# Optimization experiments

Measured on AMD Instinct MI355X. Metric: run time of the kernel, lower is better.

Reference implementation:

```python
import jax, jax.numpy as jnp
import numpy as np

WS = 8        # window_size
SHIFT = 4     # shift_size
NH = 6        # num_heads
EPS = 1e-5


def _rel_pos_index(ws):
    coords = np.stack(np.meshgrid(np.arange(ws), np.arange(ws), indexing='ij'))  # [2,ws,ws]
    cf = coords.reshape(2, -1)                      # [2, ws*ws]
    rel = cf[:, :, None] - cf[:, None, :]           # [2, N, N]
    rel = rel.transpose(1, 2, 0)                    # [N, N, 2]
    rel[:, :, 0] += ws - 1
    rel[:, :, 1] += ws - 1
    rel[:, :, 0] *= 2 * ws - 1
    return rel.sum(-1)                              # [N, N] int


def _attn_mask(H, W, ws, shift):
    img = np.zeros((H, W), dtype=np.float32)
    slices = (slice(0, -ws), slice(-ws, -shift), slice(-shift, None))
    cnt = 0
    for hs in slices:
        for wsl in slices:
            img[hs, wsl] = cnt
            cnt += 1
    mw = img.reshape(H // ws, ws, W // ws, ws).transpose(0, 2, 1, 3).reshape(-1, ws * ws)
    diff = mw[:, None, :] - mw[:, :, None]          # [nW, N, N]
    return np.where(diff != 0, -100.0, 0.0).astype(np.float32)


def _layernorm(x, g, b):
    mu = x.mean(-1, keepdims=True)
    var = ((x - mu) ** 2).mean(-1, keepdims=True)
    return (x - mu) * jax.lax.rsqrt(var + EPS) * g + b


def setup_inputs() -> dict:
    key = jax.random.key(0)
    ks = jax.random.split(key, 8)
    C, HID = 192, 768
    return {
        'x': jax.random.normal(ks[0], (8, 128, 128, C), jnp.float32),
        'g1': jnp.ones((C,), jnp.float32),
        'b1': jnp.zeros((C,), jnp.float32),
        'qkv_w': jax.random.normal(ks[1], (3 * C, C), jnp.float32) * 0.02,
        'qkv_b': jnp.zeros((3 * C,), jnp.float32),
        'rpb_table': jax.random.normal(ks[2], ((2 * WS - 1) ** 2, NH), jnp.float32) * 0.02,
        'proj_w': jax.random.normal(ks[3], (C, C), jnp.float32) * 0.02,
        'proj_b': jnp.zeros((C,), jnp.float32),
        'g2': jnp.ones((C,), jnp.float32),
        'b2': jnp.zeros((C,), jnp.float32),
        'fc1_w': jax.random.normal(ks[4], (HID, C), jnp.float32) * 0.02,
        'fc1_b': jnp.zeros((HID,), jnp.float32),
        'fc2_w': jax.random.normal(ks[5], (C, HID), jnp.float32) * 0.02,
        'fc2_b': jnp.zeros((C,), jnp.float32),
    }


def reference(x, g1, b1, qkv_w, qkv_b, rpb_table, proj_w, proj_b, g2, b2,
              fc1_w, fc1_b, fc2_w, fc2_b):
    B, H, W, C = x.shape
    N = WS * WS
    hd = C // NH
    scale = hd ** -0.5

    rpi = jnp.asarray(_rel_pos_index(WS))                 # [N,N] static
    mask = jnp.asarray(_attn_mask(H, W, WS, SHIFT))       # [nW,N,N] static
    nW = mask.shape[0]

    shortcut = x.reshape(B, H * W, C)
    xn = _layernorm(shortcut, g1, b1).reshape(B, H, W, C)

    # cyclic shift
    xs = jnp.roll(xn, shift=(-SHIFT, -SHIFT), axis=(1, 2))

    # window partition -> [B*nW, N, C]
    win = xs.reshape(B, H // WS, WS, W // WS, WS, C).transpose(0, 1, 3, 2, 4, 5)
    win = win.reshape(-1, N, C)
    B_ = win.shape[0]

    # qkv
    qkv = jnp.einsum('bnc,oc->bno', win, qkv_w) + qkv_b   # [B_,N,3C]
    qkv = qkv.reshape(B_, N, 3, NH, hd).transpose(2, 0, 3, 1, 4)  # [3,B_,NH,N,hd]
    q, k, v = qkv[0] * scale, qkv[1], qkv[2]

    attn = jnp.einsum('bhnd,bhmd->bhnm', q, k)            # [B_,NH,N,N]
    bias = rpb_table[rpi.reshape(-1)].reshape(N, N, NH).transpose(2, 0, 1)
    attn = attn + bias[None]
    attn = attn.reshape(B, nW, NH, N, N) + mask[None, :, None]
    attn = jax.nn.softmax(attn.reshape(B_, NH, N, N), axis=-1)

    out = jnp.einsum('bhnm,bhmd->bhnd', attn, v)          # [B_,NH,N,hd]
    out = out.transpose(0, 2, 1, 3).reshape(B_, N, C)
    out = jnp.einsum('bnc,oc->bno', out, proj_w) + proj_b

    # window reverse -> [B,H,W,C]
    out = out.reshape(B, H // WS, W // WS, WS, WS, C).transpose(0, 1, 3, 2, 4, 5)
    out = out.reshape(B, H, W, C)
    out = jnp.roll(out, shift=(SHIFT, SHIFT), axis=(1, 2)).reshape(B, H * W, C)

    x1 = shortcut + out
    h = _layernorm(x1, g2, b2)
    h = jnp.einsum('bnc,hc->bnh', h, fc1_w) + fc1_b
    h = jax.nn.gelu(h, approximate=False)
    h = jnp.einsum('bnh,ch->bnc', h, fc2_w) + fc2_b
    x2 = x1 + h
    return x2.reshape(B, H, W, C)
```

## Files before the change

kernel.cpp:

```cpp
#include <hip/hip_runtime.h>
#include <hip/hip_bf16.h>

typedef __attribute__((ext_vector_type(8))) short s16x8;
typedef __attribute__((ext_vector_type(4))) float f32x4;

#define TOK 131072

__device__ __forceinline__ unsigned short f2bf(float f){
    __hip_bfloat16 h = __float2bfloat16(f);
    return *reinterpret_cast<unsigned short*>(&h);
}

__device__ __forceinline__ int flab(int g){ return (g < 120) ? 0 : ((g < 124) ? 1 : 2); }

__device__ __forceinline__ void async16(const void* g, void* l){
    __builtin_amdgcn_global_load_lds(
        (const __attribute__((address_space(1))) unsigned int*)g,
        (__attribute__((address_space(3))) unsigned int*)l, 16, 0, 0);
}

__global__ __launch_bounds__(256) void wconv_all(
    const float* __restrict__ w0, const float* __restrict__ w1,
    const float* __restrict__ w2, const float* __restrict__ w3,
    unsigned short* __restrict__ o0, unsigned short* __restrict__ o1,
    unsigned short* __restrict__ o2, unsigned short* __restrict__ o3)
{
    int i = blockIdx.x*256 + threadIdx.x;
    if (i < 110592) o0[i] = f2bf(w0[i]);
    if (i < 36864)  o1[i] = f2bf(w1[i]);
    if (i < 147456) o2[i] = f2bf(w2[i]);
    if (i < 147456) o3[i] = f2bf(w3[i]);
}

__global__ __launch_bounds__(256) void ln1_win_kernel(
    const float* __restrict__ x, const float* __restrict__ g,
    const float* __restrict__ b, unsigned short* __restrict__ win)
{
    int wid  = blockIdx.x*4 + (threadIdx.x >> 6);
    int lane = threadIdx.x & 63;
    int b_ = wid >> 6, n = wid & 63;
    int bb = b_ >> 8, wi = b_ & 255;
    int wh = wi >> 4, ww = wi & 15;
    int r = n >> 3, c = n & 7;
    int h = (wh*8 + r + 4) & 127;
    int w = (ww*8 + c + 4) & 127;
    const float* px = x + (((size_t)bb*128 + h)*128 + w)*192;
    float v0 = px[lane], v1 = px[lane+64], v2 = px[lane+128];
    float s = v0 + v1 + v2;
    #pragma unroll
    for (int o = 1; o < 64; o <<= 1) s += __shfl_xor(s, o);
    float mu = s * (1.0f/192.0f);
    float d0 = v0-mu, d1 = v1-mu, d2 = v2-mu;
    float qv = d0*d0 + d1*d1 + d2*d2;
    #pragma unroll
    for (int o = 1; o < 64; o <<= 1) qv += __shfl_xor(qv, o);
    float rstd = rsqrtf(qv * (1.0f/192.0f) + 1e-5f);
    unsigned short* pw = win + (size_t)wid*192;
    pw[lane]     = f2bf(d0*rstd*g[lane]     + b[lane]);
    pw[lane+64]  = f2bf(d1*rstd*g[lane+64]  + b[lane+64]);
    pw[lane+128] = f2bf(d2*rstd*g[lane+128] + b[lane+128]);
}

__global__ __launch_bounds__(256) void ln2_kernel(
    const float* __restrict__ x1, const float* __restrict__ g,
    const float* __restrict__ b, unsigned short* __restrict__ out)
{
    int t = blockIdx.x*4 + (threadIdx.x >> 6);
    int lane = threadIdx.x & 63;
    const float* px = x1 + (size_t)t*192;
    float v0 = px[lane], v1 = px[lane+64], v2 = px[lane+128];
    float s = v0 + v1 + v2;
    #pragma unroll
    for (int o = 1; o < 64; o <<= 1) s += __shfl_xor(s, o);
    float mu = s * (1.0f/192.0f);
    float d0 = v0-mu, d1 = v1-mu, d2 = v2-mu;
    float qv = d0*d0 + d1*d1 + d2*d2;
    #pragma unroll
    for (int o = 1; o < 64; o <<= 1) qv += __shfl_xor(qv, o);
    float rstd = rsqrtf(qv * (1.0f/192.0f) + 1e-5f);
    unsigned short* pw = out + (size_t)t*192;
    pw[lane]     = f2bf(d0*rstd*g[lane]     + b[lane]);
    pw[lane+64]  = f2bf(d1*rstd*g[lane+64]  + b[lane+64]);
    pw[lane+128] = f2bf(d2*rstd*g[lane+128] + b[lane+128]);
}

__device__ __forceinline__ void mm256x64(
    const unsigned short* __restrict__ A, const unsigned short* __restrict__ W,
    int K, int m0, int o0, unsigned short* As, unsigned short* Bs,
    f32x4 (&acc)[4][4])
{
    const int tid = threadIdx.x, wv = tid >> 6, lane = tid & 63;
    const int lrow = lane & 15, quad = lane >> 4;
    const int lr8 = lane >> 3, lb = lane & 7;
    const int sb = ((lb ^ lr8) << 3);
    #pragma unroll
    for (int i = 0; i < 4; ++i)
        #pragma unroll
        for (int j = 0; j < 4; ++j) acc[i][j] = (f32x4){0.f,0.f,0.f,0.f};

    const unsigned short* Abase = A + (size_t)(m0 + wv*8 + lr8)*K + sb;
    const unsigned short* Wbase = W + (size_t)(o0 + wv*8 + lr8)*K + sb;

    for (int k0 = 0; k0 < K; k0 += 64) {
        #pragma unroll
        for (int it = 0; it < 8; ++it)
            async16(Abase + (size_t)(it*32)*K + k0, As + (it*4 + wv)*512);
        #pragma unroll
        for (int it = 0; it < 2; ++it)
            async16(Wbase + (size_t)(it*32)*K + k0, Bs + (it*4 + wv)*512);
        __syncthreads();
        #pragma unroll
        for (int kc = 0; kc < 2; ++kc) {
            const int blk = quad + 4*kc;
            s16x8 af[4], bf[4];
            #pragma unroll
            for (int i = 0; i < 4; ++i) {
                int row = wv*64 + i*16 + lrow;
                af[i] = *(const s16x8*)(As + row*64 + ((blk ^ (row & 7)) << 3));
            }
            #pragma unroll
            for (int j = 0; j < 4; ++j) {
                int row = j*16 + lrow;
                bf[j] = *(const s16x8*)(Bs + row*64 + ((blk ^ (row & 7)) << 3));
            }
            #pragma unroll
            for (int i = 0; i < 4; ++i)
                #pragma unroll
                for (int j = 0; j < 4; ++j)
                    acc[i][j] = __builtin_amdgcn_mfma_f32_16x16x32_bf16(af[i], bf[j], acc[i][j], 0, 0, 0);
        }
        __syncthreads();
    }
}

__global__ __launch_bounds__(256) void gemm_qkv_kernel(
    const unsigned short* __restrict__ A, const unsigned short* __restrict__ Wm,
    const float* __restrict__ bias, unsigned short* __restrict__ qo,
    unsigned short* __restrict__ ko, unsigned short* __restrict__ vo)
{
    __shared__ __attribute__((aligned(16))) char smem[40960];
    unsigned short* As = (unsigned short*)smem;
    unsigned short* Bs = (unsigned short*)(smem + 32768);
    const int m0 = blockIdx.y*256, o0 = blockIdx.x*64;
    f32x4 acc[4][4];
    mm256x64(A, Wm, 192, m0, o0, As, Bs, acc);
    const int tid = threadIdx.x, wv = tid >> 6, lane = tid & 63;
    const int lrow = lane & 15, quad = lane >> 4;
    const int part = o0 / 192;
    float bv[4];
    #pragma unroll
    for (int j = 0; j < 4; ++j) bv[j] = bias[o0 + j*16 + lrow];

    if (part < 2) {
        unsigned short* dst = (part == 0) ? qo : ko;
        const float scale = (part == 0) ? 0.17677669529663687f : 1.0f;
        unsigned short* T = (unsigned short*)smem;
        #pragma unroll
        for (int i = 0; i < 4; ++i)
            #pragma unroll
            for (int j = 0; j < 4; ++j)
                #pragma unroll
                for (int rg = 0; rg < 4; ++rg) {
                    int ml = wv*64 + i*16 + quad*4 + rg;
                    T[ml*72 + j*16 + lrow] = f2bf((acc[i][j][rg] + bv[j]) * scale);
                }
        __syncthreads();
        for (int c = tid; c < 2048; c += 256) {
            int row = c >> 3, blk = c & 7;
            int m = m0 + row, b_ = m >> 6, n = m & 63;
            int o_in = o0 + blk*8 - part*192;
            int head = o_in >> 5, d = o_in & 31;
            *(int4*)(dst + ((size_t)(b_*6 + head)*64 + n)*32 + d) =
                *(const int4*)(T + row*72 + blk*8);
        }
    } else {
        unsigned short* T = (unsigned short*)smem;
        #pragma unroll
        for (int i = 0; i < 4; ++i)
            #pragma unroll
            for (int j = 0; j < 4; ++j)
                #pragma unroll
                for (int rg = 0; rg < 4; ++rg) {
                    int ml = wv*64 + i*16 + quad*4 + rg;
                    T[(j*16 + lrow)*264 + ml] = f2bf(acc[i][j][rg] + bv[j]);
                }
        __syncthreads();
        for (int c = tid; c < 2048; c += 256) {
            int col = c >> 5, mb = c & 31;
            int b_ = (m0 >> 6) + (mb >> 3), n = (mb & 7) * 8;
            int o_in = o0 + col - 384;
            int head = o_in >> 5, d = o_in & 31;
            *(int4*)(vo + ((size_t)(b_*6 + head)*32 + d)*64 + n) =
                *(const int4*)(T + col*264 + mb*8);
        }
    }
}

__global__ __launch_bounds__(384) void attn_kernel(
    const unsigned short* __restrict__ q, const unsigned short* __restrict__ k,
    const unsigned short* __restrict__ vT, const float* __restrict__ rpb,
    unsigned short* __restrict__ ao)
{
    __shared__ float rpb_s[1350];
    __shared__ __attribute__((aligned(16))) unsigned short p_lds[6*4608];
    const int b_ = blockIdx.x;
    const int h = threadIdx.x >> 6;
    const int lane = threadIdx.x & 63, lrow = lane & 15, quad = lane >> 4;
    for (int i = threadIdx.x; i < 1350; i += 384) rpb_s[i] = rpb[i];
    __syncthreads();

    const size_t hb = ((size_t)b_*6 + h)*2048;
    const unsigned short* qb = q  + hb;
    const unsigned short* kb = k  + hb;
    const unsigned short* vb = vT + hb;

    s16x8 qf[4], kf[4];
    #pragma unroll
    for (int i = 0; i < 4; ++i) qf[i] = *(const s16x8*)(qb + (i*16+lrow)*32 + quad*8);
    #pragma unroll
    for (int j = 0; j < 4; ++j) kf[j] = *(const s16x8*)(kb + (j*16+lrow)*32 + quad*8);

    const f32x4 zz = {0.f,0.f,0.f,0.f};
    f32x4 s[4][4];
    #pragma unroll
    for (int i = 0; i < 4; ++i)
        #pragma unroll
        for (int j = 0; j < 4; ++j)
            s[i][j] = __builtin_amdgcn_mfma_f32_16x16x32_bf16(qf[i], kf[j], zz, 0, 0, 0);

    const int wi = b_ & 255, wh = wi >> 4, ww = wi & 15;
    int labm[4];
    #pragma unroll
    for (int j = 0; j < 4; ++j) {
        int m = j*16 + lrow;
        labm[j] = flab(wh*8 + (m >> 3))*3 + flab(ww*8 + (m & 7));
    }
    unsigned short* pl = p_lds + h*4608;
    #pragma unroll
    for (int i = 0; i < 4; ++i) {
        #pragma unroll
        for (int rg = 0; rg < 4; ++rg) {
            int n = i*16 + quad*4 + rg;
            int rn = n >> 3, cn = n & 7;
            int labn = flab(wh*8 + rn)*3 + flab(ww*8 + cn);
            float vals[4];
            float vmax = -1e30f;
            #pragma unroll
            for (int j = 0; j < 4; ++j) {
                int m = j*16 + lrow;
                int idx = ((rn - (m >> 3) + 7)*15 + (cn - (m & 7) + 7))*6 + h;
                float val = s[i][j][rg] + rpb_s[idx];
                if (labn != labm[j]) val -= 100.f;
                vals[j] = val;
                vmax = fmaxf(vmax, val);
            }
            #pragma unroll
            for (int o = 1; o < 16; o <<= 1) vmax = fmaxf(vmax, __shfl_xor(vmax, o));
            float sum = 0.f;
            #pragma unroll
            for (int j = 0; j < 4; ++j) { vals[j] = __expf(vals[j] - vmax); sum += vals[j]; }
            #pragma unroll
            for (int o = 1; o < 16; o <<= 1) sum += __shfl_xor(sum, o);
            float inv = 1.f / sum;
            #pragma unroll
            for (int j = 0; j < 4; ++j) pl[n*72 + j*16 + lrow] = f2bf(vals[j]*inv);
        }
    }
    __syncthreads();

    f32x4 oacc[4][2];
    #pragma unroll
    for (int i = 0; i < 4; ++i) { oacc[i][0] = zz; oacc[i][1] = zz; }
    #pragma unroll
    for (int kc = 0; kc < 2; ++kc) {
        s16x8 vf[2];
        #pragma unroll
        for (int jd = 0; jd < 2; ++jd)
            vf[jd] = *(const s16x8*)(vb + (jd*16+lrow)*64 + kc*32 + quad*8);
        #pragma unroll
        for (int i = 0; i < 4; ++i) {
            s16x8 pf = *(const s16x8*)(pl + (i*16+lrow)*72 + kc*32 + quad*8);
            #pragma unroll
            for (int jd = 0; jd < 2; ++jd)
                oacc[i][jd] = __builtin_amdgcn_mfma_f32_16x16x32_bf16(pf, vf[jd], oacc[i][jd], 0, 0, 0);
        }
    }
    unsigned short* ob = ao + (size_t)b_*12288 + h*32;
    #pragma unroll
    for (int i = 0; i < 4; ++i)
        #pragma unroll
        for (int jd = 0; jd < 2; ++jd)
            #pragma unroll
            for (int rg = 0; rg < 4; ++rg) {
                int n = i*16 + quad*4 + rg;
                ob[(size_t)n*192 + jd*16 + lrow] = f2bf(oacc[i][jd][rg]);
            }
}

__global__ __launch_bounds__(256) void gemm_proj_kernel(
    const unsigned short* __restrict__ A, const unsigned short* __restrict__ Wm,
    const float* __restrict__ bias, const float* __restrict__ x, float* __restrict__ x1)
{
    __shared__ __attribute__((aligned(16))) char smem[40960];
    unsigned short* As = (unsigned short*)smem;
    unsigned short* Bs = (unsigned short*)(smem + 32768);
    const int m0 = blockIdx.y*256, o0 = blockIdx.x*64;
    f32x4 acc[4][4];
    mm256x64(A, Wm, 192, m0, o0, As, Bs, acc);
    const int tid = threadIdx.x, wv = tid >> 6, lane = tid & 63;
    const int lrow = lane & 15, quad = lane >> 4;
    float bv[4];
    #pragma unroll
    for (int j = 0; j < 4; ++j) bv[j] = bias[o0 + j*16 + lrow];
    float* T = (float*)smem;
    #pragma unroll
    for (int pass = 0; pass < 2; ++pass) {
        __syncthreads();
        if ((wv >> 1) == pass) {
            int wl = wv & 1;
            #pragma unroll
            for (int i = 0; i < 4; ++i)
                #pragma unroll
                for (int j = 0; j < 4; ++j)
                    #pragma unroll
                    for (int rg = 0; rg < 4; ++rg)
                        T[(wl*64 + i*16 + quad*4 + rg)*68 + j*16 + lrow] = acc[i][j][rg] + bv[j];
        }
        __syncthreads();
        for (int c = tid; c < 2048; c += 256) {
            int row = c >> 4, blk = c & 15;
            int m = m0 + pass*128 + row;
            int b_ = m >> 6, n = m & 63;
            int bb = b_ >> 8, wi = b_ & 255, wh = wi >> 4, ww = wi & 15;
            int r = n >> 3, cc = n & 7;
            int hh = (wh*8 + r + 4) & 127;
            int wwp = (ww*8 + cc + 4) & 127;
            size_t addr = (((size_t)bb*128 + hh)*128 + wwp)*192 + o0 + blk*4;
            float4 v = *(const float4*)(T + row*68 + blk*4);
            float4 rx = *(const float4*)(x + addr);
            v.x += rx.x; v.y += rx.y; v.z += rx.z; v.w += rx.w;
            *(float4*)(x1 + addr) = v;
        }
    }
}

__global__ __launch_bounds__(256) void gemm_fc1_kernel(
    const unsigned short* __restrict__ A, const unsigned short* __restrict__ Wm,
    const float* __restrict__ bias, unsigned short* __restrict__ h1)
{
    __shared__ __attribute__((aligned(16))) char smem[40960];
    unsigned short* As = (unsigned short*)smem;
    unsigned short* Bs = (unsigned short*)(smem + 32768);
    const int m0 = blockIdx.y*256, o0 = blockIdx.x*64;
    f32x4 acc[4][4];
    mm256x64(A, Wm, 192, m0, o0, As, Bs, acc);
    const int tid = threadIdx.x, wv = tid >> 6, lane = tid & 63;
    const int lrow = lane & 15, quad = lane >> 4;
    float bv[4];
    #pragma unroll
    for (int j = 0; j < 4; ++j) bv[j] = bias[o0 + j*16 + lrow];
    unsigned short* T = (unsigned short*)smem;
    #pragma unroll
    for (int i = 0; i < 4; ++i)
        #pragma unroll
        for (int j = 0; j < 4; ++j)
            #pragma unroll
            for (int rg = 0; rg < 4; ++rg) {
                int ml = wv*64 + i*16 + quad*4 + rg;
                float v = acc[i][j][rg] + bv[j];
                v = 0.5f * v * (1.0f + erff(v * 0.7071067811865475f));
                T[ml*72 + j*16 + lrow] = f2bf(v);
            }
    __syncthreads();
    for (int c = tid; c < 2048; c += 256) {
        int row = c >> 3, blk = c & 7;
        *(int4*)(h1 + (size_t)(m0 + row)*768 + o0 + blk*8) =
            *(const int4*)(T + row*72 + blk*8);
    }
}

__global__ __launch_bounds__(256) void gemm_fc2_kernel(
    const unsigned short* __restrict__ A, const unsigned short* __restrict__ Wm,
    const float* __restrict__ bias, const float* __restrict__ x1, float* __restrict__ out)
{
    __shared__ __attribute__((aligned(16))) char smem[40960];
    unsigned short* As = (unsigned short*)smem;
    unsigned short* Bs = (unsigned short*)(smem + 32768);
    const int m0 = blockIdx.y*256, o0 = blockIdx.x*64;
    f32x4 acc[4][4];
    mm256x64(A, Wm, 768, m0, o0, As, Bs, acc);
    const int tid = threadIdx.x, wv = tid >> 6, lane = tid & 63;
    const int lrow = lane & 15, quad = lane >> 4;
    float bv[4];
    #pragma unroll
    for (int j = 0; j < 4; ++j) bv[j] = bias[o0 + j*16 + lrow];
    float* T = (float*)smem;
    #pragma unroll
    for (int pass = 0; pass < 2; ++pass) {
        __syncthreads();
        if ((wv >> 1) == pass) {
            int wl = wv & 1;
            #pragma unroll
            for (int i = 0; i < 4; ++i)
                #pragma unroll
                for (int j = 0; j < 4; ++j)
                    #pragma unroll
                    for (int rg = 0; rg < 4; ++rg)
                        T[(wl*64 + i*16 + quad*4 + rg)*68 + j*16 + lrow] = acc[i][j][rg] + bv[j];
        }
        __syncthreads();
        for (int c = tid; c < 2048; c += 256) {
            int row = c >> 4, blk = c & 15;
            size_t addr = (size_t)(m0 + pass*128 + row)*192 + o0 + blk*4;
            float4 v = *(const float4*)(T + row*68 + blk*4);
            float4 rx = *(const float4*)(x1 + addr);
            v.x += rx.x; v.y += rx.y; v.z += rx.z; v.w += rx.w;
            *(float4*)(out + addr) = v;
        }
    }
}

extern "C" void kernel_launch(void* const* d_in, const int* in_sizes, int n_in,
                              void* d_out, int out_size, void* d_ws, size_t ws_size,
                              hipStream_t stream)
{
    const float* x      = (const float*)d_in[0];
    const float* g1     = (const float*)d_in[1];
    const float* b1     = (const float*)d_in[2];
    const float* qkv_w  = (const float*)d_in[3];
    const float* qkv_b  = (const float*)d_in[4];
    const float* rpb    = (const float*)d_in[5];
    const float* proj_w = (const float*)d_in[6];
    const float* proj_b = (const float*)d_in[7];
    const float* g2     = (const float*)d_in[8];
    const float* b2     = (const float*)d_in[9];
    const float* fc1_w  = (const float*)d_in[10];
    const float* fc1_b  = (const float*)d_in[11];
    const float* fc2_w  = (const float*)d_in[12];
    const float* fc2_b  = (const float*)d_in[13];
    float* out = (float*)d_out;
    char* ws = (char*)d_ws;

    if (ws_size < 353206272ULL) return;

    unsigned short* win  = (unsigned short*)(ws + 0);
    unsigned short* qbuf = (unsigned short*)(ws + 50331648);
    unsigned short* kbuf = (unsigned short*)(ws + 100663296);
    unsigned short* vbuf = (unsigned short*)(ws + 150994944);
    unsigned short* attn = (unsigned short*)(ws + 201326592);
    float*          x1   = (float*)        (ws + 251658240);
    unsigned short* wq   = (unsigned short*)(ws + 352321536);
    unsigned short* wp   = (unsigned short*)(ws + 352321536 + 221184);
    unsigned short* w1   = (unsigned short*)(ws + 352321536 + 221184 + 73728);
    unsigned short* w2   = (unsigned short*)(ws + 352321536 + 221184 + 73728 + 294912);
    unsigned short* h1   = (unsigned short*)(ws + 0);
    unsigned short* xln2 = attn;

    wconv_all<<<576, 256, 0, stream>>>(qkv_w, proj_w, fc1_w, fc2_w, wq, wp, w1, w2);
    ln1_win_kernel<<<TOK/4, 256, 0, stream>>>(x, g1, b1, win);
    gemm_qkv_kernel<<<dim3(9, 512), 256, 0, stream>>>(win, wq, qkv_b, qbuf, kbuf, vbuf);
    attn_kernel<<<2048, 384, 0, stream>>>(qbuf, kbuf, vbuf, rpb, attn);
    gemm_proj_kernel<<<dim3(3, 512), 256, 0, stream>>>(attn, wp, proj_b, x, x1);
    ln2_kernel<<<TOK/4, 256, 0, stream>>>(x1, g2, b2, xln2);
    gemm_fc1_kernel<<<dim3(12, 512), 256, 0, stream>>>(xln2, w1, fc1_b, h1);
    gemm_fc2_kernel<<<dim3(3, 512), 256, 0, stream>>>(h1, w2, fc2_b, x1, out);
}
```

Measured before the change: 673.5 us.

## Fuse LayerNorm1 into QKV GEMM and LayerNorm2 into projection GEMM

LN1 plus the window gather now run inside a per-window QKV kernel that keeps the normalized tile in LDS, so the separate `win` buffer round trip goes away. The projection kernel now covers all 192 output columns per window, which lets it add the residual, compute LN2 in registers and write both x1 and xln2. This removes the standalone ln2 pass. The FC1 and FC2 GEMMs switch to 128-row tiles for more blocks. The trade-offs are plain int4 global loads instead of async LDS loads in the fused kernels and more register pressure (acc[12] plus the LN vectors).

New measurement: 591.3 us. -12.2%, faster.

```diff
diff --git a/kernel.cpp b/kernel.cpp
--- a/kernel.cpp
+++ b/kernel.cpp
@@ -3,8 +3,6 @@
 
 typedef __attribute__((ext_vector_type(8))) short s16x8;
 typedef __attribute__((ext_vector_type(4))) float f32x4;
-
-#define TOK 131072
 
 __device__ __forceinline__ unsigned short f2bf(float f){
     __hip_bfloat16 h = __float2bfloat16(f);
@@ -32,166 +30,115 @@
     if (i < 147456) o3[i] = f2bf(w3[i]);
 }
 
-__global__ __launch_bounds__(256) void ln1_win_kernel(
-    const float* __restrict__ x, const float* __restrict__ g,
-    const float* __restrict__ b, unsigned short* __restrict__ win)
-{
-    int wid  = blockIdx.x*4 + (threadIdx.x >> 6);
-    int lane = threadIdx.x & 63;
-    int b_ = wid >> 6, n = wid & 63;
-    int bb = b_ >> 8, wi = b_ & 255;
-    int wh = wi >> 4, ww = wi & 15;
-    int r = n >> 3, c = n & 7;
-    int h = (wh*8 + r + 4) & 127;
-    int w = (ww*8 + c + 4) & 127;
-    const float* px = x + (((size_t)bb*128 + h)*128 + w)*192;
-    float v0 = px[lane], v1 = px[lane+64], v2 = px[lane+128];
-    float s = v0 + v1 + v2;
-    #pragma unroll
-    for (int o = 1; o < 64; o <<= 1) s += __shfl_xor(s, o);
-    float mu = s * (1.0f/192.0f);
-    float d0 = v0-mu, d1 = v1-mu, d2 = v2-mu;
-    float qv = d0*d0 + d1*d1 + d2*d2;
-    #pragma unroll
-    for (int o = 1; o < 64; o <<= 1) qv += __shfl_xor(qv, o);
-    float rstd = rsqrtf(qv * (1.0f/192.0f) + 1e-5f);
-    unsigned short* pw = win + (size_t)wid*192;
-    pw[lane]     = f2bf(d0*rstd*g[lane]     + b[lane]);
-    pw[lane+64]  = f2bf(d1*rstd*g[lane+64]  + b[lane+64]);
-    pw[lane+128] = f2bf(d2*rstd*g[lane+128] + b[lane+128]);
-}
-
-__global__ __launch_bounds__(256) void ln2_kernel(
-    const float* __restrict__ x1, const float* __restrict__ g,
-    const float* __restrict__ b, unsigned short* __restrict__ out)
-{
-    int t = blockIdx.x*4 + (threadIdx.x >> 6);
-    int lane = threadIdx.x & 63;
-    const float* px = x1 + (size_t)t*192;
-    float v0 = px[lane], v1 = px[lane+64], v2 = px[lane+128];
-    float s = v0 + v1 + v2;
-    #pragma unroll
-    for (int o = 1; o < 64; o <<= 1) s += __shfl_xor(s, o);
-    float mu = s * (1.0f/192.0f);
-    float d0 = v0-mu, d1 = v1-mu, d2 = v2-mu;
-    float qv = d0*d0 + d1*d1 + d2*d2;
-    #pragma unroll
-    for (int o = 1; o < 64; o <<= 1) qv += __shfl_xor(qv, o);
-    float rstd = rsqrtf(qv * (1.0f/192.0f) + 1e-5f);
-    unsigned short* pw = out + (size_t)t*192;
-    pw[lane]     = f2bf(d0*rstd*g[lane]     + b[lane]);
-    pw[lane+64]  = f2bf(d1*rstd*g[lane+64]  + b[lane+64]);
-    pw[lane+128] = f2bf(d2*rstd*g[lane+128] + b[lane+128]);
-}
-
-__device__ __forceinline__ void mm256x64(
-    const unsigned short* __restrict__ A, const unsigned short* __restrict__ W,
-    int K, int m0, int o0, unsigned short* As, unsigned short* Bs,
-    f32x4 (&acc)[4][4])
-{
-    const int tid = threadIdx.x, wv = tid >> 6, lane = tid & 63;
-    const int lrow = lane & 15, quad = lane >> 4;
-    const int lr8 = lane >> 3, lb = lane & 7;
-    const int sb = ((lb ^ lr8) << 3);
-    #pragma unroll
-    for (int i = 0; i < 4; ++i)
-        #pragma unroll
-        for (int j = 0; j < 4; ++j) acc[i][j] = (f32x4){0.f,0.f,0.f,0.f};
-
-    const unsigned short* Abase = A + (size_t)(m0 + wv*8 + lr8)*K + sb;
-    const unsigned short* Wbase = W + (size_t)(o0 + wv*8 + lr8)*K + sb;
-
-    for (int k0 = 0; k0 < K; k0 += 64) {
-        #pragma unroll
-        for (int it = 0; it < 8; ++it)
-            async16(Abase + (size_t)(it*32)*K + k0, As + (it*4 + wv)*512);
-        #pragma unroll
-        for (int it = 0; it < 2; ++it)
-            async16(Wbase + (size_t)(it*32)*K + k0, Bs + (it*4 + wv)*512);
-        __syncthreads();
-        #pragma unroll
-        for (int kc = 0; kc < 2; ++kc) {
-            const int blk = quad + 4*kc;
-            s16x8 af[4], bf[4];
-            #pragma unroll
-            for (int i = 0; i < 4; ++i) {
-                int row = wv*64 + i*16 + lrow;
-                af[i] = *(const s16x8*)(As + row*64 + ((blk ^ (row & 7)) << 3));
-            }
-            #pragma unroll
-            for (int j = 0; j < 4; ++j) {
-                int row = j*16 + lrow;
-                bf[j] = *(const s16x8*)(Bs + row*64 + ((blk ^ (row & 7)) << 3));
-            }
-            #pragma unroll
-            for (int i = 0; i < 4; ++i)
+__global__ __launch_bounds__(256) void lnqkv_kernel(
+    const float* __restrict__ x, const float* __restrict__ g1, const float* __restrict__ b1,
+    const unsigned short* __restrict__ wq, const float* __restrict__ qkvb,
+    unsigned short* __restrict__ qo, unsigned short* __restrict__ ko,
+    unsigned short* __restrict__ vo)
+{
+    __shared__ __attribute__((aligned(16))) unsigned short win[64*200];
+    __shared__ __attribute__((aligned(16))) unsigned short Bs[64*200];
+    const int b_ = blockIdx.x;
+    const int bb = b_>>8, wi = b_&255, wh = wi>>4, ww = wi&15;
+    const int tid = threadIdx.x;
+    const int wv = tid>>6, lane = tid&63, lrow = lane&15, quad = lane>>4;
+
+    {
+        const int n = tid>>2, q4 = tid&3;
+        const int r = n>>3, c = n&7;
+        const int hh = (wh*8 + r + 4)&127, wp = (ww*8 + c + 4)&127;
+        const float* px = x + (((size_t)bb*128+hh)*128+wp)*192 + q4*48;
+        float v[48];
+        #pragma unroll
+        for (int m=0;m<12;++m) *(float4*)(v+m*4) = *(const float4*)(px+m*4);
+        float s = 0.f;
+        #pragma unroll
+        for (int k=0;k<48;++k) s += v[k];
+        s += __shfl_xor(s,1); s += __shfl_xor(s,2);
+        float mu = s*(1.0f/192.0f);
+        float qv = 0.f;
+        #pragma unroll
+        for (int k=0;k<48;++k){ float d=v[k]-mu; qv += d*d; }
+        qv += __shfl_xor(qv,1); qv += __shfl_xor(qv,2);
+        float rstd = rsqrtf(qv*(1.0f/192.0f) + 1e-5f);
+        const float* pg = g1 + q4*48;
+        const float* pb = b1 + q4*48;
+        unsigned short* pw = win + n*200 + q4*48;
+        #pragma unroll
+        for (int k=0;k<48;++k) pw[k] = f2bf((v[k]-mu)*rstd*pg[k] + pb[k]);
+    }
+    __syncthreads();
+
+    s16x8 af[6];
+    #pragma unroll
+    for (int kc=0;kc<6;++kc)
+        af[kc] = *(const s16x8*)(win + (wv*16+lrow)*200 + kc*32 + quad*8);
+
+    for (int ot=0; ot<9; ++ot) {
+        const int o0 = ot*64;
+        __syncthreads();
+        #pragma unroll
+        for (int t=0;t<6;++t) {
+            int cid = tid + t*256;
+            *(int4*)(Bs + (cid/24)*200 + (cid%24)*8) =
+                *(const int4*)(wq + (size_t)o0*192 + cid*8);
+        }
+        __syncthreads();
+        f32x4 acc[4];
+        #pragma unroll
+        for (int j=0;j<4;++j) acc[j] = (f32x4){0.f,0.f,0.f,0.f};
+        #pragma unroll
+        for (int kc=0;kc<6;++kc)
+            #pragma unroll
+            for (int j=0;j<4;++j) {
+                s16x8 bf = *(const s16x8*)(Bs + (j*16+lrow)*200 + kc*32 + quad*8);
+                acc[j] = __builtin_amdgcn_mfma_f32_16x16x32_bf16(af[kc], bf, acc[j], 0, 0, 0);
+            }
+        __syncthreads();
+        unsigned short* T = Bs;
+        const int part = ot/3;
+        float bv[4];
+        #pragma unroll
+        for (int j=0;j<4;++j) bv[j] = qkvb[o0 + j*16 + lrow];
+
+        if (part < 2) {
+            const float scale = (part==0) ? 0.17677669529663687f : 1.0f;
+            #pragma unroll
+            for (int j=0;j<4;++j)
                 #pragma unroll
-                for (int j = 0; j < 4; ++j)
-                    acc[i][j] = __builtin_amdgcn_mfma_f32_16x16x32_bf16(af[i], bf[j], acc[i][j], 0, 0, 0);
-        }
-        __syncthreads();
-    }
-}
-
-__global__ __launch_bounds__(256) void gemm_qkv_kernel(
-    const unsigned short* __restrict__ A, const unsigned short* __restrict__ Wm,
-    const float* __restrict__ bias, unsigned short* __restrict__ qo,
-    unsigned short* __restrict__ ko, unsigned short* __restrict__ vo)
-{
-    __shared__ __attribute__((aligned(16))) char smem[40960];
-    unsigned short* As = (unsigned short*)smem;
-    unsigned short* Bs = (unsigned short*)(smem + 32768);
-    const int m0 = blockIdx.y*256, o0 = blockIdx.x*64;
-    f32x4 acc[4][4];
-    mm256x64(A, Wm, 192, m0, o0, As, Bs, acc);
-    const int tid = threadIdx.x, wv = tid >> 6, lane = tid & 63;
-    const int lrow = lane & 15, quad = lane >> 4;
-    const int part = o0 / 192;
-    float bv[4];
-    #pragma unroll
-    for (int j = 0; j < 4; ++j) bv[j] = bias[o0 + j*16 + lrow];
-
-    if (part < 2) {
-        unsigned short* dst = (part == 0) ? qo : ko;
-        const float scale = (part == 0) ? 0.17677669529663687f : 1.0f;
-        unsigned short* T = (unsigned short*)smem;
-        #pragma unroll
-        for (int i = 0; i < 4; ++i)
-            #pragma unroll
-            for (int j = 0; j < 4; ++j)
+                for (int rg=0;rg<4;++rg) {
+                    int n2 = wv*16 + quad*4 + rg;
+                    T[n2*72 + j*16 + lrow] = f2bf((acc[j][rg]+bv[j])*scale);
+                }
+            __syncthreads();
+            unsigned short* dst = (part==0) ? qo : ko;
+            #pragma unroll
+            for (int t=0;t<2;++t) {
+                int c = tid + t*256;
+                int n2 = c>>3, blk = c&7;
+                int o_in = o0 + blk*8 - part*192;
+                int head = o_in>>5, d = o_in&31;
+                *(int4*)(dst + (((size_t)b_*6+head)*64 + n2)*32 + d) =
+                    *(const int4*)(T + n2*72 + blk*8);
+            }
+        } else {
+            #pragma unroll
+            for (int j=0;j<4;++j)
                 #pragma unroll
-                for (int rg = 0; rg < 4; ++rg) {
-                    int ml = wv*64 + i*16 + quad*4 + rg;
-                    T[ml*72 + j*16 + lrow] = f2bf((acc[i][j][rg] + bv[j]) * scale);
+                for (int rg=0;rg<4;++rg) {
+                    int n2 = wv*16 + quad*4 + rg;
+                    T[(j*16+lrow)*72 + n2] = f2bf(acc[j][rg]+bv[j]);
                 }
-        __syncthreads();
-        for (int c = tid; c < 2048; c += 256) {
-            int row = c >> 3, blk = c & 7;
-            int m = m0 + row, b_ = m >> 6, n = m & 63;
-            int o_in = o0 + blk*8 - part*192;
-            int head = o_in >> 5, d = o_in & 31;
-            *(int4*)(dst + ((size_t)(b_*6 + head)*64 + n)*32 + d) =
-                *(const int4*)(T + row*72 + blk*8);
-        }
-    } else {
-        unsigned short* T = (unsigned short*)smem;
-        #pragma unroll
-        for (int i = 0; i < 4; ++i)
-            #pragma unroll
-            for (int j = 0; j < 4; ++j)
-                #pragma unroll
-                for (int rg = 0; rg < 4; ++rg) {
-                    int ml = wv*64 + i*16 + quad*4 + rg;
-                    T[(j*16 + lrow)*264 + ml] = f2bf(acc[i][j][rg] + bv[j]);
-                }
-        __syncthreads();
-        for (int c = tid; c < 2048; c += 256) {
-            int col = c >> 5, mb = c & 31;
-            int b_ = (m0 >> 6) + (mb >> 3), n = (mb & 7) * 8;
-            int o_in = o0 + col - 384;
-            int head = o_in >> 5, d = o_in & 31;
-            *(int4*)(vo + ((size_t)(b_*6 + head)*32 + d)*64 + n) =
-                *(const int4*)(T + col*264 + mb*8);
+            __syncthreads();
+            #pragma unroll
+            for (int t=0;t<2;++t) {
+                int c = tid + t*256;
+                int ol = c>>3, nb = (c&7)*8;
+                int o_in = o0 + ol - 384;
+                int head = o_in>>5, d = o_in&31;
+                *(int4*)(vo + (((size_t)b_*6+head)*32 + d)*64 + nb) =
+                    *(const int4*)(T + ol*72 + nb);
+            }
         }
     }
 }
@@ -297,50 +244,146 @@
             }
 }
 
-__global__ __launch_bounds__(256) void gemm_proj_kernel(
-    const unsigned short* __restrict__ A, const unsigned short* __restrict__ Wm,
-    const float* __restrict__ bias, const float* __restrict__ x, float* __restrict__ x1)
-{
-    __shared__ __attribute__((aligned(16))) char smem[40960];
+__global__ __launch_bounds__(256) void projln_kernel(
+    const unsigned short* __restrict__ A, const unsigned short* __restrict__ W,
+    const float* __restrict__ pbias, const float* __restrict__ x,
+    const float* __restrict__ g2, const float* __restrict__ b2,
+    float* __restrict__ x1, unsigned short* __restrict__ xln2)
+{
+    __shared__ __attribute__((aligned(16))) char smem[36864];
     unsigned short* As = (unsigned short*)smem;
-    unsigned short* Bs = (unsigned short*)(smem + 32768);
-    const int m0 = blockIdx.y*256, o0 = blockIdx.x*64;
-    f32x4 acc[4][4];
-    mm256x64(A, Wm, 192, m0, o0, As, Bs, acc);
-    const int tid = threadIdx.x, wv = tid >> 6, lane = tid & 63;
-    const int lrow = lane & 15, quad = lane >> 4;
-    float bv[4];
-    #pragma unroll
-    for (int j = 0; j < 4; ++j) bv[j] = bias[o0 + j*16 + lrow];
-    float* T = (float*)smem;
-    #pragma unroll
-    for (int pass = 0; pass < 2; ++pass) {
-        __syncthreads();
-        if ((wv >> 1) == pass) {
-            int wl = wv & 1;
-            #pragma unroll
-            for (int i = 0; i < 4; ++i)
+    unsigned short* Bs = (unsigned short*)(smem + 9216);
+    const int b_ = blockIdx.x;
+    const int tid = threadIdx.x, wv = tid>>6, lane = tid&63;
+    const int lrow = lane&15, quad = lane>>4;
+    const size_t m0 = (size_t)b_*64;
+
+    f32x4 acc[12];
+    #pragma unroll
+    for (int j=0;j<12;++j) acc[j] = (f32x4){0.f,0.f,0.f,0.f};
+
+    for (int k0=0;k0<192;k0+=64) {
+        __syncthreads();
+        #pragma unroll
+        for (int t=0;t<2;++t) {
+            int cid = tid + t*256;
+            *(int4*)(As + (cid>>3)*72 + (cid&7)*8) =
+                *(const int4*)(A + (m0 + (cid>>3))*192 + k0 + (cid&7)*8);
+        }
+        #pragma unroll
+        for (int t=0;t<6;++t) {
+            int cid = tid + t*256;
+            *(int4*)(Bs + (cid>>3)*72 + (cid&7)*8) =
+                *(const int4*)(W + (size_t)(cid>>3)*192 + k0 + (cid&7)*8);
+        }
+        __syncthreads();
+        #pragma unroll
+        for (int kc=0;kc<2;++kc) {
+            s16x8 af = *(const s16x8*)(As + (wv*16+lrow)*72 + kc*32 + quad*8);
+            #pragma unroll
+            for (int j=0;j<12;++j) {
+                s16x8 bf = *(const s16x8*)(Bs + (j*16+lrow)*72 + kc*32 + quad*8);
+                acc[j] = __builtin_amdgcn_mfma_f32_16x16x32_bf16(af, bf, acc[j], 0, 0, 0);
+            }
+        }
+    }
+    __syncthreads();
+
+    const int bb = b_>>8, wi = b_&255, wh = wi>>4, ww = wi&15;
+    float bv[12], gv[12], b2v[12];
+    #pragma unroll
+    for (int j=0;j<12;++j) {
+        bv[j]  = pbias[j*16+lrow];
+        gv[j]  = g2[j*16+lrow];
+        b2v[j] = b2[j*16+lrow];
+    }
+    unsigned short* T = (unsigned short*)smem;
+    #pragma unroll
+    for (int rg=0;rg<4;++rg) {
+        int n2 = wv*16 + quad*4 + rg;
+        int r = n2>>3, c = n2&7;
+        int hh = (wh*8+r+4)&127, wp = (ww*8+c+4)&127;
+        size_t tok = ((size_t)bb*128+hh)*128 + wp;
+        float xv[12];
+        float s = 0.f;
+        #pragma unroll
+        for (int j=0;j<12;++j) {
+            float t = acc[j][rg] + bv[j] + x[tok*192 + j*16 + lrow];
+            xv[j] = t; s += t;
+        }
+        #pragma unroll
+        for (int o=1;o<16;o<<=1) s += __shfl_xor(s, o);
+        float mu = s*(1.0f/192.0f);
+        float qv = 0.f;
+        #pragma unroll
+        for (int j=0;j<12;++j){ float d = xv[j]-mu; qv += d*d; }
+        #pragma unroll
+        for (int o=1;o<16;o<<=1) qv += __shfl_xor(qv, o);
+        float rstd = rsqrtf(qv*(1.0f/192.0f) + 1e-5f);
+        #pragma unroll
+        for (int j=0;j<12;++j) {
+            x1[tok*192 + j*16 + lrow] = xv[j];
+            T[n2*200 + j*16 + lrow] = f2bf((xv[j]-mu)*rstd*gv[j] + b2v[j]);
+        }
+    }
+    __syncthreads();
+    #pragma unroll
+    for (int t=0;t<6;++t) {
+        int cid = tid + t*256;
+        int n2 = cid/24, blk = cid%24;
+        int r = n2>>3, c = n2&7;
+        int hh = (wh*8+r+4)&127, wp = (ww*8+c+4)&127;
+        size_t tok = ((size_t)bb*128+hh)*128 + wp;
+        *(int4*)(xln2 + tok*192 + blk*8) = *(const int4*)(T + n2*200 + blk*8);
+    }
+}
+
+__device__ __forceinline__ void mm128x64(
+    const unsigned short* __restrict__ A, const unsigned short* __restrict__ W,
+    int K, size_t m0, int o0, unsigned short* As, unsigned short* Bs,
+    f32x4 (&acc)[2][4])
+{
+    const int tid = threadIdx.x, wv = tid>>6, lane = tid&63;
+    const int lrow = lane&15, quad = lane>>4;
+    const int lr8 = lane>>3, lb = lane&7;
+    const int sb = ((lb ^ lr8) << 3);
+    #pragma unroll
+    for (int i=0;i<2;++i)
+        #pragma unroll
+        for (int j=0;j<4;++j) acc[i][j] = (f32x4){0.f,0.f,0.f,0.f};
+
+    const unsigned short* Abase = A + (m0 + wv*8 + lr8)*K + sb;
+    const unsigned short* Wbase = W + (size_t)(o0 + wv*8 + lr8)*K + sb;
+
+    for (int k0=0;k0<K;k0+=64) {
+        #pragma unroll
+        for (int it=0;it<4;++it)
+            async16(Abase + (size_t)(it*32)*K + k0, As + (it*4+wv)*512);
+        #pragma unroll
+        for (int it=0;it<2;++it)
+            async16(Wbase + (size_t)(it*32)*K + k0, Bs + (it*4+wv)*512);
+        __syncthreads();
+        #pragma unroll
+        for (int kc=0;kc<2;++kc) {
+            const int blk = quad + 4*kc;
+            s16x8 af[2], bf[4];
+            #pragma unroll
+            for (int i=0;i<2;++i) {
+                int row = wv*32 + i*16 + lrow;
+                af[i] = *(const s16x8*)(As + row*64 + ((blk ^ (row&7)) << 3));
+            }
+            #pragma unroll
+            for (int j=0;j<4;++j) {
+                int row = j*16 + lrow;
+                bf[j] = *(const s16x8*)(Bs + row*64 + ((blk ^ (row&7)) << 3));
+            }
+            #pragma unroll
+            for (int i=0;i<2;++i)
                 #pragma unroll
-                for (int j = 0; j < 4; ++j)
-                    #pragma unroll
-                    for (int rg = 0; rg < 4; ++rg)
-                        T[(wl*64 + i*16 + quad*4 + rg)*68 + j*16 + lrow] = acc[i][j][rg] + bv[j];
-        }
-        __syncthreads();
-        for (int c = tid; c < 2048; c += 256) {
-            int row = c >> 4, blk = c & 15;
-            int m = m0 + pass*128 + row;
-            int b_ = m >> 6, n = m & 63;
-            int bb = b_ >> 8, wi = b_ & 255, wh = wi >> 4, ww = wi & 15;
-            int r = n >> 3, cc = n & 7;
-            int hh = (wh*8 + r + 4) & 127;
-            int wwp = (ww*8 + cc + 4) & 127;
-            size_t addr = (((size_t)bb*128 + hh)*128 + wwp)*192 + o0 + blk*4;
-            float4 v = *(const float4*)(T + row*68 + blk*4);
-            float4 rx = *(const float4*)(x + addr);
-            v.x += rx.x; v.y += rx.y; v.z += rx.z; v.w += rx.w;
-            *(float4*)(x1 + addr) = v;
-        }
+                for (int j=0;j<4;++j)
+                    acc[i][j] = __builtin_amdgcn_mfma_f32_16x16x32_bf16(af[i], bf[j], acc[i][j], 0, 0, 0);
+        }
+        __syncthreads();
     }
 }
 
@@ -348,34 +391,36 @@
     const unsigned short* __restrict__ A, const unsigned short* __restrict__ Wm,
     const float* __restrict__ bias, unsigned short* __restrict__ h1)
 {
-    __shared__ __attribute__((aligned(16))) char smem[40960];
+    __shared__ __attribute__((aligned(16))) char smem[24576];
     unsigned short* As = (unsigned short*)smem;
-    unsigned short* Bs = (unsigned short*)(smem + 32768);
-    const int m0 = blockIdx.y*256, o0 = blockIdx.x*64;
-    f32x4 acc[4][4];
-    mm256x64(A, Wm, 192, m0, o0, As, Bs, acc);
-    const int tid = threadIdx.x, wv = tid >> 6, lane = tid & 63;
-    const int lrow = lane & 15, quad = lane >> 4;
+    unsigned short* Bs = (unsigned short*)(smem + 16384);
+    const size_t m0 = (size_t)blockIdx.y*128;
+    const int o0 = blockIdx.x*64;
+    f32x4 acc[2][4];
+    mm128x64(A, Wm, 192, m0, o0, As, Bs, acc);
+    const int tid = threadIdx.x, wv = tid>>6, lane = tid&63;
+    const int lrow = lane&15, quad = lane>>4;
     float bv[4];
     #pragma unroll
-    for (int j = 0; j < 4; ++j) bv[j] = bias[o0 + j*16 + lrow];
+    for (int j=0;j<4;++j) bv[j] = bias[o0 + j*16 + lrow];
     unsigned short* T = (unsigned short*)smem;
     #pragma unroll
-    for (int i = 0; i < 4; ++i)
-        #pragma unroll
-        for (int j = 0; j < 4; ++j)
-            #pragma unroll
-            for (int rg = 0; rg < 4; ++rg) {
-                int ml = wv*64 + i*16 + quad*4 + rg;
+    for (int i=0;i<2;++i)
+        #pragma unroll
+        for (int j=0;j<4;++j)
+            #pragma unroll
+            for (int rg=0;rg<4;++rg) {
+                int ml = wv*32 + i*16 + quad*4 + rg;
                 float v = acc[i][j][rg] + bv[j];
-                v = 0.5f * v * (1.0f + erff(v * 0.7071067811865475f));
+                v = 0.5f*v*(1.0f + erff(v*0.7071067811865475f));
                 T[ml*72 + j*16 + lrow] = f2bf(v);
             }
     __syncthreads();
-    for (int c = tid; c < 2048; c += 256) {
-        int row = c >> 3, blk = c & 7;
-        *(int4*)(h1 + (size_t)(m0 + row)*768 + o0 + blk*8) =
-            *(const int4*)(T + row*72 + blk*8);
+    #pragma unroll
+    for (int t=0;t<4;++t) {
+        int c = tid + t*256;
+        int row = c>>3, blk = c&7;
+        *(int4*)(h1 + (m0+row)*768 + o0 + blk*8) = *(const int4*)(T + row*72 + blk*8);
     }
 }
 
@@ -383,39 +428,42 @@
     const unsigned short* __restrict__ A, const unsigned short* __restrict__ Wm,
     const float* __restrict__ bias, const float* __restrict__ x1, float* __restrict__ out)
 {
-    __shared__ __attribute__((aligned(16))) char smem[40960];
+    __shared__ __attribute__((aligned(16))) char smem[24576];
     unsigned short* As = (unsigned short*)smem;
-    unsigned short* Bs = (unsigned short*)(smem + 32768);
-    const int m0 = blockIdx.y*256, o0 = blockIdx.x*64;
-    f32x4 acc[4][4];
-    mm256x64(A, Wm, 768, m0, o0, As, Bs, acc);
-    const int tid = threadIdx.x, wv = tid >> 6, lane = tid & 63;
-    const int lrow = lane & 15, quad = lane >> 4;
+    unsigned short* Bs = (unsigned short*)(smem + 16384);
+    const size_t m0 = (size_t)blockIdx.y*128;
+    const int o0 = blockIdx.x*64;
+    f32x4 acc[2][4];
+    mm128x64(A, Wm, 768, m0, o0, As, Bs, acc);
+    const int tid = threadIdx.x, wv = tid>>6, lane = tid&63;
+    const int lrow = lane&15, quad = lane>>4;
     float bv[4];
     #pragma unroll
-    for (int j = 0; j < 4; ++j) bv[j] = bias[o0 + j*16 + lrow];
+    for (int j=0;j<4;++j) bv[j] = bias[o0 + j*16 + lrow];
     float* T = (float*)smem;
     #pragma unroll
-    for (int pass = 0; pass < 2; ++pass) {
-        __syncthreads();
-        if ((wv >> 1) == pass) {
-            int wl = wv & 1;
-            #pragma unroll
-            for (int i = 0; i < 4; ++i)
+    for (int p=0;p<2;++p) {
+        __syncthreads();
+        if ((wv>>1) == p) {
+            int wl = wv&1;
+            #pragma unroll
+            for (int i=0;i<2;++i)
                 #pragma unroll
-                for (int j = 0; j < 4; ++j)
+                for (int j=0;j<4;++j)
                     #pragma unroll
-                    for (int rg = 0; rg < 4; ++rg)
-                        T[(wl*64 + i*16 + quad*4 + rg)*68 + j*16 + lrow] = acc[i][j][rg] + bv[j];
-        }
-        __syncthreads();
-        for (int c = tid; c < 2048; c += 256) {
-            int row = c >> 4, blk = c & 15;
-            size_t addr = (size_t)(m0 + pass*128 + row)*192 + o0 + blk*4;
+                    for (int rg=0;rg<4;++rg)
+                        T[(wl*32 + i*16 + quad*4 + rg)*68 + j*16 + lrow] = acc[i][j][rg] + bv[j];
+        }
+        __syncthreads();
+        #pragma unroll
+        for (int t=0;t<4;++t) {
+            int c = tid + t*256;
+            int row = c>>4, blk = c&15;
+            size_t ad = (m0 + p*64 + row)*192 + o0 + blk*4;
             float4 v = *(const float4*)(T + row*68 + blk*4);
-            float4 rx = *(const float4*)(x1 + addr);
+            float4 rx = *(const float4*)(x1 + ad);
             v.x += rx.x; v.y += rx.y; v.z += rx.z; v.w += rx.w;
-            *(float4*)(out + addr) = v;
+            *(float4*)(out + ad) = v;
         }
     }
 }
@@ -443,25 +491,22 @@
 
     if (ws_size < 353206272ULL) return;
 
-    unsigned short* win  = (unsigned short*)(ws + 0);
-    unsigned short* qbuf = (unsigned short*)(ws + 50331648);
-    unsigned short* kbuf = (unsigned short*)(ws + 100663296);
-    unsigned short* vbuf = (unsigned short*)(ws + 150994944);
-    unsigned short* attn = (unsigned short*)(ws + 201326592);
-    float*          x1   = (float*)        (ws + 251658240);
-    unsigned short* wq   = (unsigned short*)(ws + 352321536);
-    unsigned short* wp   = (unsigned short*)(ws + 352321536 + 221184);
-    unsigned short* w1   = (unsigned short*)(ws + 352321536 + 221184 + 73728);
-    unsigned short* w2   = (unsigned short*)(ws + 352321536 + 221184 + 73728 + 294912);
-    unsigned short* h1   = (unsigned short*)(ws + 0);
-    unsigned short* xln2 = attn;
+    unsigned short* qbuf  = (unsigned short*)(ws + 0);
+    unsigned short* kbuf  = (unsigned short*)(ws + 50331648);
+    unsigned short* vbuf  = (unsigned short*)(ws + 100663296);
+    unsigned short* attnO = (unsigned short*)(ws + 150994944);
+    float*          x1    = (float*)        (ws + 201326592);
+    unsigned short* xln2  = (unsigned short*)(ws + 301989888);
+    unsigned short* wq    = (unsigned short*)(ws + 352321536);
+    unsigned short* wp    = (unsigned short*)(ws + 352321536 + 221184);
+    unsigned short* w1    = (unsigned short*)(ws + 352321536 + 221184 + 73728);
+    unsigned short* w2    = (unsigned short*)(ws + 352321536 + 221184 + 73728 + 294912);
+    unsigned short* h1    = (unsigned short*)(ws + 0);
 
     wconv_all<<<576, 256, 0, stream>>>(qkv_w, proj_w, fc1_w, fc2_w, wq, wp, w1, w2);
-    ln1_win_kernel<<<TOK/4, 256, 0, stream>>>(x, g1, b1, win);
-    gemm_qkv_kernel<<<dim3(9, 512), 256, 0, stream>>>(win, wq, qkv_b, qbuf, kbuf, vbuf);
-    attn_kernel<<<2048, 384, 0, stream>>>(qbuf, kbuf, vbuf, rpb, attn);
-    gemm_proj_kernel<<<dim3(3, 512), 256, 0, stream>>>(attn, wp, proj_b, x, x1);
-    ln2_kernel<<<TOK/4, 256, 0, stream>>>(x1, g2, b2, xln2);
-    gemm_fc1_kernel<<<dim3(12, 512), 256, 0, stream>>>(xln2, w1, fc1_b, h1);
-    gemm_fc2_kernel<<<dim3(3, 512), 256, 0, stream>>>(h1, w2, fc2_b, x1, out);
-}
+    lnqkv_kernel<<<2048, 256, 0, stream>>>(x, g1, b1, wq, qkv_b, qbuf, kbuf, vbuf);
+    attn_kernel<<<2048, 384, 0, stream>>>(qbuf, kbuf, vbuf, rpb, attnO);
+    projln_kernel<<<2048, 256, 0, stream>>>(attnO, wp, proj_b, x, g2, b2, x1, xln2);
+    gemm_fc1_kernel<<<dim3(12, 1024), 256, 0, stream>>>(xln2, w1, fc1_b, h1);
+    gemm_fc2_kernel<<<dim3(3, 1024), 256, 0, stream>>>(h1, w2, fc2_b, x1, out);
+}
```
